# Optimization experiments

Hardware: AMD Instinct MI355X
Metric: run time of the kernel (lower is better)

The kernel has to match this reference:

```python
import jax, jax.numpy as jnp
import numpy as np

THRESHOLD = 50.0
LEVELS = 3
NORMALIZE = True


def _haar_step(x):
    """One level of 2D Haar DWT on [B,H,W] (H,W even).
    Equivalent to pywt.dwt2(x, 'haar') up to sign conventions, which do not
    affect the sparsity loss (it depends only on |coeff|)."""
    a = x[:, 0::2, 0::2]
    b = x[:, 0::2, 1::2]
    c = x[:, 1::2, 0::2]
    d = x[:, 1::2, 1::2]
    cA = (a + b + c + d) * 0.5
    cH = (a + b - c - d) * 0.5  # vertical-highpass detail
    cV = (a - b + c - d) * 0.5  # horizontal-highpass detail
    cD = (a - b - c + d) * 0.5  # diagonal detail
    return cA, cH, cV, cD


def _band_loss(c, thr):
    # L1 distance between coeffs and their soft-thresholded version:
    # |c - ST(c, thr)| = min(|c|, thr) elementwise; mean over batch+spatial
    # equals the torch per-sample l1_loss averaged over the batch.
    return jnp.mean(jnp.minimum(jnp.abs(c), thr))


def setup_inputs() -> dict:
    key = jax.random.key(0)
    pred = jax.random.uniform(key, (32, 1, 1024, 1024), dtype=jnp.float32)
    return {"pred": pred}


def reference(pred):
    x = pred[:, 0]  # [B, H, W]
    total = jnp.float32(0.0)
    for s in range(1, LEVELS + 1):
        x, cH, cV, cD = _haar_step(x)
        # s=1 is the finest detail band; pywt's coeffs[level_idx=1] is the
        # coarsest, so map: level_idx = LEVELS - s + 1.
        level_idx = LEVELS - s + 1
        thr = THRESHOLD / (2.0 ** (level_idx - 1))
        if NORMALIZE:
            thr = thr / 255.0
        level_weight = 1.0 / level_idx
        level_loss = (_band_loss(cH, thr) + _band_loss(cV, thr) + _band_loss(cD, thr)) / 3.0
        total = total + level_weight * level_loss
    return total
```

## Files before the change

kernel.cpp:

```cpp
#include <hip/hip_runtime.h>

#define IMG_W 1024
#define IMG_H 1024
#define NBATCH 32

__device__ __forceinline__ void haar_quad(float a, float b, float c, float d,
                                          float thr, float& cA, float& lsum) {
    float s1 = a + b, s2 = c + d;
    float d1 = a - b, d2 = c - d;
    cA = (s1 + s2) * 0.5f;
    float cH = (s1 - s2) * 0.5f;
    float cV = (d1 + d2) * 0.5f;
    float cD = (d1 - d2) * 0.5f;
    lsum += fminf(fabsf(cH), thr) + fminf(fabsf(cV), thr) + fminf(fabsf(cD), thr);
}

__global__ __launch_bounds__(256)
void WaveletSparsityLoss_34746285424743_kernel(const float* __restrict__ pred,
                                               float* __restrict__ out) {
    int tid = blockIdx.x * blockDim.x + threadIdx.x;
    int batch = tid >> 14;
    int t     = tid & 16383;
    int tr    = t >> 7;
    int tc    = t & 127;

    const float* img = pred + (size_t)batch * (IMG_W * IMG_H);
    int r0 = tr * 8;
    int c0 = tc * 8;

    const float thr1 = 50.0f / 4.0f / 255.0f;
    const float thr2 = 50.0f / 2.0f / 255.0f;
    const float thr3 = 50.0f / 255.0f;

    float l1 = 0.0f, l2 = 0.0f, l3 = 0.0f;
    float cA1[4][4];

    #pragma unroll
    for (int i = 0; i < 4; ++i) {
        const float4* rowA = reinterpret_cast<const float4*>(
            img + (size_t)(r0 + 2 * i) * IMG_W + c0);
        const float4* rowB = reinterpret_cast<const float4*>(
            img + (size_t)(r0 + 2 * i + 1) * IMG_W + c0);
        float4 a0 = rowA[0], a1 = rowA[1];
        float4 b0 = rowB[0], b1 = rowB[1];
        haar_quad(a0.x, a0.y, b0.x, b0.y, thr1, cA1[i][0], l1);
        haar_quad(a0.z, a0.w, b0.z, b0.w, thr1, cA1[i][1], l1);
        haar_quad(a1.x, a1.y, b1.x, b1.y, thr1, cA1[i][2], l1);
        haar_quad(a1.z, a1.w, b1.z, b1.w, thr1, cA1[i][3], l1);
    }

    float cA2[2][2];
    #pragma unroll
    for (int i = 0; i < 2; ++i) {
        haar_quad(cA1[2*i][0], cA1[2*i][1], cA1[2*i+1][0], cA1[2*i+1][1],
                  thr2, cA2[i][0], l2);
        haar_quad(cA1[2*i][2], cA1[2*i][3], cA1[2*i+1][2], cA1[2*i+1][3],
                  thr2, cA2[i][1], l2);
    }

    float cA3;
    haar_quad(cA2[0][0], cA2[0][1], cA2[1][0], cA2[1][1], thr3, cA3, l3);
    (void)cA3;

    const float C1 = 1.0f / (3.0f * 3.0f * 8388608.0f);
    const float C2 = 1.0f / (2.0f * 3.0f * 2097152.0f);
    const float C3 = 1.0f / (3.0f * 524288.0f);
    float v = l1 * C1 + l2 * C2 + l3 * C3;

    #pragma unroll
    for (int off = 32; off > 0; off >>= 1)
        v += __shfl_down(v, off, 64);

    __shared__ float wsum[4];
    int lane = threadIdx.x & 63;
    int wid  = threadIdx.x >> 6;
    if (lane == 0) wsum[wid] = v;
    __syncthreads();
    if (threadIdx.x == 0) {
        float s = wsum[0] + wsum[1] + wsum[2] + wsum[3];
        atomicAdd(out, s);
    }
}

extern "C" void kernel_launch(void* const* d_in, const int* in_sizes, int n_in,
                              void* d_out, int out_size, void* d_ws, size_t ws_size,
                              hipStream_t stream) {
    const float* pred = (const float*)d_in[0];
    float* out = (float*)d_out;

    hipMemsetAsync(out, 0, sizeof(float), stream);

    WaveletSparsityLoss_34746285424743_kernel<<<2048, 256, 0, stream>>>(pred, out);
}
```

Baseline: 187.1 us.

## Coalesce row loads per strip and replace atomics with two-stage reduction

Each block now handles an 8-row strip of one image, and each lane loads one float4 from each of the 8 rows, so a wavefront reads fully contiguous row segments instead of strided 8x8 tiles. The level-3 Haar step pairs neighbouring lanes with a shuffle, and the level-3 weight is halved because both lanes of a pair add the same term. The global atomic and the memset are replaced by per-block partial sums written to workspace and a single-block second kernel that reduces them. This is meant to improve DRAM access coalescing and drop atomic contention, at the cost of an extra kernel launch.

```diff
diff --git a/kernel.cpp b/kernel.cpp
--- a/kernel.cpp
+++ b/kernel.cpp
@@ -3,6 +3,7 @@
 #define IMG_W 1024
 #define IMG_H 1024
 #define NBATCH 32
+#define STAGE1_BLOCKS (NBATCH * (IMG_H / 8))
 
 __device__ __forceinline__ void haar_quad(float a, float b, float c, float d,
                                           float thr, float& cA, float& lsum) {
@@ -16,70 +17,84 @@
 }
 
 __global__ __launch_bounds__(256)
-void WaveletSparsityLoss_34746285424743_kernel(const float* __restrict__ pred,
-                                               float* __restrict__ out) {
-    int tid = blockIdx.x * blockDim.x + threadIdx.x;
-    int batch = tid >> 14;
-    int t     = tid & 16383;
-    int tr    = t >> 7;
-    int tc    = t & 127;
+void wavelet_stage1(const float* __restrict__ pred, float* __restrict__ partial) {
+    int batch = blockIdx.x >> 7;
+    int strip = blockIdx.x & 127;
+    int lane  = threadIdx.x & 63;
+    int wid   = threadIdx.x >> 6;
 
     const float* img = pred + (size_t)batch * (IMG_W * IMG_H);
-    int r0 = tr * 8;
-    int c0 = tc * 8;
+    int r0 = strip * 8;
+    int c0 = wid * 256 + lane * 4;
 
     const float thr1 = 50.0f / 4.0f / 255.0f;
     const float thr2 = 50.0f / 2.0f / 255.0f;
     const float thr3 = 50.0f / 255.0f;
 
-    float l1 = 0.0f, l2 = 0.0f, l3 = 0.0f;
-    float cA1[4][4];
-
+    float4 v[8];
     #pragma unroll
-    for (int i = 0; i < 4; ++i) {
-        const float4* rowA = reinterpret_cast<const float4*>(
-            img + (size_t)(r0 + 2 * i) * IMG_W + c0);
-        const float4* rowB = reinterpret_cast<const float4*>(
-            img + (size_t)(r0 + 2 * i + 1) * IMG_W + c0);
-        float4 a0 = rowA[0], a1 = rowA[1];
-        float4 b0 = rowB[0], b1 = rowB[1];
-        haar_quad(a0.x, a0.y, b0.x, b0.y, thr1, cA1[i][0], l1);
-        haar_quad(a0.z, a0.w, b0.z, b0.w, thr1, cA1[i][1], l1);
-        haar_quad(a1.x, a1.y, b1.x, b1.y, thr1, cA1[i][2], l1);
-        haar_quad(a1.z, a1.w, b1.z, b1.w, thr1, cA1[i][3], l1);
+    for (int i = 0; i < 8; ++i) {
+        v[i] = *reinterpret_cast<const float4*>(
+            img + (size_t)(r0 + i) * IMG_W + c0);
     }
 
-    float cA2[2][2];
+    float l1 = 0.0f, l2 = 0.0f, l3 = 0.0f;
+
+    float cA1[4][2];
     #pragma unroll
-    for (int i = 0; i < 2; ++i) {
-        haar_quad(cA1[2*i][0], cA1[2*i][1], cA1[2*i+1][0], cA1[2*i+1][1],
-                  thr2, cA2[i][0], l2);
-        haar_quad(cA1[2*i][2], cA1[2*i][3], cA1[2*i+1][2], cA1[2*i+1][3],
-                  thr2, cA2[i][1], l2);
+    for (int p = 0; p < 4; ++p) {
+        float4 t = v[2 * p], b = v[2 * p + 1];
+        haar_quad(t.x, t.y, b.x, b.y, thr1, cA1[p][0], l1);
+        haar_quad(t.z, t.w, b.z, b.w, thr1, cA1[p][1], l1);
     }
 
+    float cA2[2];
+    #pragma unroll
+    for (int q = 0; q < 2; ++q) {
+        haar_quad(cA1[2 * q][0], cA1[2 * q][1],
+                  cA1[2 * q + 1][0], cA1[2 * q + 1][1], thr2, cA2[q], l2);
+    }
+
+    float pb = __shfl_xor(cA2[0], 1, 64);
+    float pd = __shfl_xor(cA2[1], 1, 64);
     float cA3;
-    haar_quad(cA2[0][0], cA2[0][1], cA2[1][0], cA2[1][1], thr3, cA3, l3);
+    haar_quad(cA2[0], pb, cA2[1], pd, thr3, cA3, l3);
     (void)cA3;
 
     const float C1 = 1.0f / (3.0f * 3.0f * 8388608.0f);
     const float C2 = 1.0f / (2.0f * 3.0f * 2097152.0f);
-    const float C3 = 1.0f / (3.0f * 524288.0f);
-    float v = l1 * C1 + l2 * C2 + l3 * C3;
+    const float C3 = 0.5f / (3.0f * 524288.0f);
+    float s = l1 * C1 + l2 * C2 + l3 * C3;
 
     #pragma unroll
     for (int off = 32; off > 0; off >>= 1)
-        v += __shfl_down(v, off, 64);
+        s += __shfl_down(s, off, 64);
+
+    __shared__ float wsum[4];
+    if (lane == 0) wsum[wid] = s;
+    __syncthreads();
+    if (threadIdx.x == 0)
+        partial[blockIdx.x] = wsum[0] + wsum[1] + wsum[2] + wsum[3];
+}
+
+__global__ __launch_bounds__(256)
+void wavelet_stage2(const float* __restrict__ partial, float* __restrict__ out) {
+    float s = 0.0f;
+    #pragma unroll
+    for (int i = 0; i < STAGE1_BLOCKS / 256; ++i)
+        s += partial[threadIdx.x + i * 256];
+
+    #pragma unroll
+    for (int off = 32; off > 0; off >>= 1)
+        s += __shfl_down(s, off, 64);
 
     __shared__ float wsum[4];
     int lane = threadIdx.x & 63;
     int wid  = threadIdx.x >> 6;
-    if (lane == 0) wsum[wid] = v;
+    if (lane == 0) wsum[wid] = s;
     __syncthreads();
-    if (threadIdx.x == 0) {
-        float s = wsum[0] + wsum[1] + wsum[2] + wsum[3];
-        atomicAdd(out, s);
-    }
+    if (threadIdx.x == 0)
+        out[0] = wsum[0] + wsum[1] + wsum[2] + wsum[3];
 }
 
 extern "C" void kernel_launch(void* const* d_in, const int* in_sizes, int n_in,
@@ -87,8 +102,8 @@
                               hipStream_t stream) {
     const float* pred = (const float*)d_in[0];
     float* out = (float*)d_out;
+    float* partial = (float*)d_ws;
 
-    hipMemsetAsync(out, 0, sizeof(float), stream);
-
-    WaveletSparsityLoss_34746285424743_kernel<<<2048, 256, 0, stream>>>(pred, out);
+    wavelet_stage1<<<STAGE1_BLOCKS, 256, 0, stream>>>(pred, partial);
+    wavelet_stage2<<<1, 256, 0, stream>>>(partial, out);
 }
```

New measurement: 185.4 us. Within noise of the previous version (-0.9%).
